# Kernel optimization log

Measured on AMD Instinct MI355X. Metric: run time of the kernel, lower is better.

Reference implementation:

```python
import jax, jax.numpy as jnp
import numpy as np

D_MODEL = 1024


def setup_inputs() -> dict:
    key = jax.random.key(0)
    ks = jax.random.split(key, 9)
    B, S, D = 4, 2048, D_MODEL
    scale = 1.0 / np.sqrt(D)
    inp = {
        "tokens": jax.random.normal(ks[0], (B, S, D), dtype=jnp.float32),
        "Wq": jax.random.normal(ks[1], (D, D), dtype=jnp.float32) * scale,
        "bq": jnp.zeros((D,), dtype=jnp.float32),
        "Wk": jax.random.normal(ks[2], (D, D), dtype=jnp.float32) * scale,
        "bk": jnp.zeros((D,), dtype=jnp.float32),
        "Wv": jax.random.normal(ks[3], (D, D), dtype=jnp.float32) * scale,
        "bv": jnp.zeros((D,), dtype=jnp.float32),
        "Wo": jax.random.normal(ks[4], (D, D), dtype=jnp.float32) * scale,
        "bo": jnp.zeros((D,), dtype=jnp.float32),
    }
    return inp


def reference(tokens, Wq, bq, Wk, bk, Wv, bv, Wo, bo):
    # use_activation=True, use_residual=True
    residual = tokens
    x = jax.nn.gelu(tokens, approximate=False)  # F.gelu default is exact (erf)
    q = jnp.einsum("bsd,de->bse", x, Wq) + bq
    k = jnp.einsum("bsd,de->bse", x, Wk) + bk
    v = jnp.einsum("bsd,de->bse", x, Wv) + bv
    scale = 1.0 / jnp.sqrt(jnp.asarray(tokens.shape[-1], dtype=tokens.dtype))
    scores = jnp.einsum("bqd,bkd->bqk", q, k) * scale  # [B,S,S]
    attn = jax.nn.softmax(scores, axis=-1)
    mixed = jnp.einsum("bqk,bkd->bqd", attn, v)
    out = jnp.einsum("bsd,de->bse", mixed, Wo) + bo
    return out + residual
```

## Files before the change

kernel.cpp:

```cpp
#include <hip/hip_runtime.h>
#include <hip/hip_bf16.h>
#include <cstdint>
#include <cstddef>

typedef unsigned short u16;
using frag_ab = __attribute__((ext_vector_type(8))) short;
using f32x4   = __attribute__((ext_vector_type(4))) float;

__device__ __forceinline__ u16 f2bf(float x) {
    __hip_bfloat16 h = __float2bfloat16(x);
    return *reinterpret_cast<u16*>(&h);
}

__device__ __forceinline__ void gload_lds16(const u16* g, u16* l) {
    __builtin_amdgcn_global_load_lds(
        (const __attribute__((address_space(1))) uint32_t*)g,
        (__attribute__((address_space(3)))       uint32_t*)l,
        16, 0, 0);
}

#define WAITV4() do { asm volatile("s_waitcnt vmcnt(4)" ::: "memory"); \
                      __builtin_amdgcn_sched_barrier(0); } while (0)
#define WAITV0() do { asm volatile("s_waitcnt vmcnt(0)" ::: "memory"); \
                      __builtin_amdgcn_sched_barrier(0); } while (0)
#define BAR()    do { asm volatile("" ::: "memory"); __builtin_amdgcn_s_barrier(); \
                      __builtin_amdgcn_sched_barrier(0); } while (0)
#define LGKMC(N) do { asm volatile("s_waitcnt lgkmcnt(" #N ")" ::: "memory"); \
                      __builtin_amdgcn_sched_barrier(0); } while (0)
#define LGKM0()  LGKMC(0)

template<int EPI, int BN_>
__global__ __launch_bounds__(512, 2)
void gemm3a(const u16* __restrict__ A, const u16* __restrict__ Bt,
            void* __restrict__ C0,
            const float* __restrict__ b0, const float* __restrict__ resid,
            int K, int lda, int ldb, int ldc,
            long long sA, long long sB, long long sC, float alpha,
            float* __restrict__ partials, int nz)
{
    constexpr int NFQ  = BN_ / 64;
    constexpr int WN   = BN_ / 2;
    constexpr int BBUF = BN_ * 64;
    __shared__ __align__(16) u16 lds[49152 + 2 * BBUF];

    const int gx  = gridDim.x;
    const int gid = blockIdx.x + gx * blockIdx.y;
    const int c   = gid & 7;
    const int idx = gid >> 3;
    const int z   = c % nz;
    const int sub = c / nz;
    const int W   = gridDim.y >> 3;
    const int mp  = sub * W + idx % W;
    const int np  = idx / W;
    const int m0  = mp * 256;
    const int n0  = np * BN_;

    A  += (long long)z * sA;
    Bt += (long long)z * sB;

    const int t    = threadIdx.x;
    const int lane = t & 63;
    const int wave = t >> 6;
    const int wm   = wave >> 1;
    const int wn   = wave & 1;

    const int r0  = t >> 3;
    const int ssw = (t & 7) ^ (r0 & 7);
    const u16* gsA_0 = A  + (size_t)(m0 +       r0) * lda + ssw * 8;
    const u16* gsA_1 = A  + (size_t)(m0 +  64 + r0) * lda + ssw * 8;
    const u16* gsA_2 = A  + (size_t)(m0 + 128 + r0) * lda + ssw * 8;
    const u16* gsA_3 = A  + (size_t)(m0 + 192 + r0) * lda + ssw * 8;
    const u16* gsB_0 = Bt + (size_t)(n0 +       r0) * ldb + ssw * 8;
    const u16* gsB_1 = Bt + (size_t)(n0 +  64 + r0) * ldb + ssw * 8;
    const u16* gsB_2 = (BN_ == 256) ? Bt + (size_t)(n0 + 128 + r0) * ldb + ssw * 8 : gsB_0;
    const u16* gsB_3 = (BN_ == 256) ? Bt + (size_t)(n0 + 192 + r0) * ldb + ssw * 8 : gsB_1;

#define STA(BUF, H, KT) do {                                                   \
    gload_lds16(((H) ? gsA_2 : gsA_0) + (size_t)(KT) * 64,                     \
                lds + (BUF) * 16384 + (H) * 8192 + t * 8);                     \
    gload_lds16(((H) ? gsA_3 : gsA_1) + (size_t)(KT) * 64,                     \
                lds + (BUF) * 16384 + (H) * 8192 + 4096 + t * 8);              \
} while (0)
#define STB(BUF, H, KT) do {                                                   \
    gload_lds16(((H) ? gsB_2 : gsB_0) + (size_t)(KT) * 64,                     \
                lds + 49152 + (BUF) * BBUF + (H) * 8192 + t * 8);              \
    gload_lds16(((H) ? gsB_3 : gsB_1) + (size_t)(KT) * 64,                     \
                lds + 49152 + (BUF) * BBUF + (H) * 8192 + 4096 + t * 8);       \
} while (0)

    const int ar   = lane & 15;
    const int ko   = lane >> 4;
    const int aoff = (wm * 64 + ar) * 64;
    const int boff = 49152 + (wn * WN + ar) * 64;
    const int as0  = ((0 + ko) ^ (ar & 7)) * 8;
    const int as1  = ((4 + ko) ^ (ar & 7)) * 8;

    frag_ab areg[2][2];
    frag_ab breg[2][NFQ][2];
    f32x4   acc[4][2 * NFQ] = {};

#define RDA3(AB, MQ) do { _Pragma("unroll") for (int mf = 0; mf < 2; ++mf) {   \
    areg[mf][0] = *(const frag_ab*)(lds + (AB) + aoff + ((MQ)*2+mf)*1024 + as0); \
    areg[mf][1] = *(const frag_ab*)(lds + (AB) + aoff + ((MQ)*2+mf)*1024 + as1); } } while (0)

#define RDB3(BO, NQ) do { _Pragma("unroll") for (int jf = 0; jf < NFQ; ++jf) { \
    breg[NQ][jf][0] = *(const frag_ab*)(lds + (BO) + boff + ((NQ)*NFQ+jf)*1024 + as0); \
    breg[NQ][jf][1] = *(const frag_ab*)(lds + (BO) + boff + ((NQ)*NFQ+jf)*1024 + as1); } } while (0)

#define MMAQ3(MQ, NQ) do { __builtin_amdgcn_s_setprio(1);                      \
    _Pragma("unroll") for (int mf = 0; mf < 2; ++mf)                           \
    _Pragma("unroll") for (int jf = 0; jf < NFQ; ++jf) {                       \
        acc[(MQ)*2+mf][(NQ)*NFQ+jf] = __builtin_amdgcn_mfma_f32_16x16x32_bf16( \
            areg[mf][0], breg[NQ][jf][0], acc[(MQ)*2+mf][(NQ)*NFQ+jf], 0,0,0); \
        acc[(MQ)*2+mf][(NQ)*NFQ+jf] = __builtin_amdgcn_mfma_f32_16x16x32_bf16( \
            areg[mf][1], breg[NQ][jf][1], acc[(MQ)*2+mf][(NQ)*NFQ+jf], 0,0,0); \
    } __builtin_amdgcn_s_setprio(0); } while (0)

    const int nk = K / 64;
    STA(0, 0, 0); STA(0, 1, 0);
    STB(0, 0, 0);
    if constexpr (BN_ == 256) STB(0, 1, 0);
    STA(1, 0, 1); STA(1, 1, 1);
    WAITV4();
    BAR();

    int ab = 0, bb = 0;
    for (int tt = 0; tt < nk; ++tt) {
        const int ab2 = (ab + 2 >= 3) ? ab - 1 : ab + 2;
        const int bb1 = bb ^ 1;
        const int tB  = (tt + 1 < nk) ? tt + 1 : nk - 1;
        const int tA  = (tt + 2 < nk) ? tt + 2 : nk - 1;
        const int AB = ab * 16384, BB = bb * BBUF;
        RDA3(AB, 0); RDB3(BB, 0);
        STB(bb1, 0, tB);
        if constexpr (BN_ == 256) LGKMC(8);
        BAR(); LGKM0(); MMAQ3(0, 0);
        RDB3(BB, 1);
        if constexpr (BN_ == 256) STB(bb1, 1, tB);
        BAR(); LGKM0(); MMAQ3(0, 1);
        RDA3(AB, 1);
        STA(ab2, 0, tA);
        BAR(); LGKM0(); MMAQ3(1, 0);
        STA(ab2, 1, tA);
        WAITV4();
        BAR(); MMAQ3(1, 1);
        ab = (ab + 1 >= 3) ? 0 : ab + 1;
        bb = bb1;
    }

    const int cr = (lane >> 4) * 4;
    const int cc = lane & 15;

    float* fl = (float*)lds;
    if constexpr (EPI == 2) {
        WAITV0();
        BAR();
        if (t < 256) {
            const float* p = partials + ((size_t)z * 2048 + m0 + t) * 16;
            float s = 0.0f;
            #pragma unroll
            for (int i = 0; i < 16; ++i) s += p[i];
            fl[t] = 1.0f / s;
        }
        BAR();
    }

    float rs[4][4];
    if constexpr (EPI == 1) {
        #pragma unroll
        for (int mi = 0; mi < 4; ++mi)
            #pragma unroll
            for (int r = 0; r < 4; ++r) rs[mi][r] = 0.0f;
    }

    #pragma unroll
    for (int mi = 0; mi < 4; ++mi) {
        const int rowb = m0 + wm * 64 + mi * 16 + cr;
        const int rloc = wm * 64 + mi * 16 + cr;
        #pragma unroll
        for (int gj = 0; gj < 2 * NFQ; ++gj) {
            const int col = n0 + wn * WN + gj * 16 + cc;
            if constexpr (EPI == 0) {
                const int plane = col >> 10;
                const int cl    = col & 1023;
                const float bvv = ((plane == 0) ? b0 : resid)[cl];
                u16* Cw = (u16*)C0 + (size_t)plane * sC;
                #pragma unroll
                for (int r = 0; r < 4; ++r)
                    Cw[(size_t)(rowb + r) * ldc + cl] = f2bf(acc[mi][gj][r] + bvv);
            } else {
                const float bvv = (EPI == 3) ? b0[col] : 0.0f;
                #pragma unroll
                for (int r = 0; r < 4; ++r) {
                    const size_t row = (size_t)(rowb + r);
                    float v = acc[mi][gj][r];
                    if (EPI == 1) { v = __expf(v * alpha); rs[mi][r] += v; }
                    if (EPI == 2) v *= fl[rloc + r];
                    v += bvv;
                    if (EPI == 3) {
                        v += resid[row * ldc + col];
                        ((float*)C0)[(size_t)z * sC + row * ldc + col] = v;
                    } else {
                        ((u16*)C0)[(size_t)z * sC + row * ldc + col] = f2bf(v);
                    }
                }
            }
        }
    }

    if constexpr (EPI == 1) {
        #pragma unroll
        for (int mi = 0; mi < 4; ++mi)
            #pragma unroll
            for (int r = 0; r < 4; ++r) {
                float s = rs[mi][r];
                s += __shfl_xor(s, 1); s += __shfl_xor(s, 2);
                s += __shfl_xor(s, 4); s += __shfl_xor(s, 8);
                rs[mi][r] = s;
            }
        if (cc == 0) {
            const int chunk = (n0 >> 7) + wn;
            #pragma unroll
            for (int mi = 0; mi < 4; ++mi) {
                const int rowb = m0 + wm * 64 + mi * 16 + cr;
                #pragma unroll
                for (int r = 0; r < 4; ++r)
                    partials[((size_t)z * 2048 + rowb + r) * 16 + chunk] = rs[mi][r];
            }
        }
    }
#undef STA
#undef STB
#undef RDA3
#undef RDB3
#undef MMAQ3
}

__global__ __launch_bounds__(256, 2)
void gemm128_v(const u16* __restrict__ A, const u16* __restrict__ Bt,
               u16* __restrict__ VT, const float* __restrict__ bv,
               int K, int lda, int ldb)
{
    constexpr int BUFSTR = 16384;
    __shared__ __align__(16) u16 lds[2 * BUFSTR];

    const int gx  = gridDim.x;
    const int nwg = gx * gridDim.y;
    const int cpx = nwg >> 3;
    int lin = blockIdx.x + gx * blockIdx.y;
    lin = (lin & 7) * cpx + (lin >> 3);
    const int m0 = (lin / gx) * 128;
    const int n0 = (lin % gx) * 128;

    const int t    = threadIdx.x;
    const int lane = t & 63;
    const int wave = t >> 6;
    const int wm   = wave >> 1;
    const int wn   = wave & 1;

    const int r0  = t >> 3;
    const int ssw = (t & 7) ^ (r0 & 7);
    const u16* gsA0_0 = A  + (size_t)(m0 +       r0) * lda + ssw * 8;
    const u16* gsA0_1 = A  + (size_t)(m0 +  32 + r0) * lda + ssw * 8;
    const u16* gsA1_0 = A  + (size_t)(m0 +  64 + r0) * lda + ssw * 8;
    const u16* gsA1_1 = A  + (size_t)(m0 +  96 + r0) * lda + ssw * 8;
    const u16* gsB0_0 = Bt + (size_t)(n0 +       r0) * ldb + ssw * 8;
    const u16* gsB0_1 = Bt + (size_t)(n0 +  32 + r0) * ldb + ssw * 8;
    const u16* gsB1_0 = Bt + (size_t)(n0 +  64 + r0) * ldb + ssw * 8;
    const u16* gsB1_1 = Bt + (size_t)(n0 +  96 + r0) * ldb + ssw * 8;

#define OPO_A 0
#define OPO_B 8192
#define STAGE(BI, OP, H, KT) do {                                              \
    gload_lds16(gs##OP##H##_0 + (size_t)(KT) * 64,                             \
                lds + (BI) * BUFSTR + OPO_##OP + (H) * 4096 + t * 8);          \
    gload_lds16(gs##OP##H##_1 + (size_t)(KT) * 64,                             \
                lds + (BI) * BUFSTR + OPO_##OP + (H) * 4096 + 2048 + t * 8);   \
} while (0)

    const int ar   = lane & 15;
    const int ko   = lane >> 4;
    const int aoff = (wm * 64 + ar) * 64;
    const int boff = OPO_B + (wn * 64 + ar) * 64;
    const int as0  = ((0 + ko) ^ (ar & 7)) * 8;
    const int as1  = ((4 + ko) ^ (ar & 7)) * 8;

    frag_ab areg[2][2];
    frag_ab breg[2][2][2];
    f32x4   acc[4][4] = {};

#define RDA(BI, MQ) do { _Pragma("unroll") for (int mf = 0; mf < 2; ++mf) {    \
    areg[mf][0] = *(const frag_ab*)(lds + (BI)*BUFSTR + aoff + ((MQ)*2+mf)*1024 + as0); \
    areg[mf][1] = *(const frag_ab*)(lds + (BI)*BUFSTR + aoff + ((MQ)*2+mf)*1024 + as1); } } while (0)

#define RDB(BI, NQ) do { _Pragma("unroll") for (int jf = 0; jf < 2; ++jf) {    \
    breg[NQ][jf][0] = *(const frag_ab*)(lds + (BI)*BUFSTR + boff + ((NQ)*2+jf)*1024 + as0); \
    breg[NQ][jf][1] = *(const frag_ab*)(lds + (BI)*BUFSTR + boff + ((NQ)*2+jf)*1024 + as1); } } while (0)

#define MMAQ(MQ, NQ) do { __builtin_amdgcn_s_setprio(1);                       \
    _Pragma("unroll") for (int mf = 0; mf < 2; ++mf)                           \
    _Pragma("unroll") for (int jf = 0; jf < 2; ++jf) {                         \
        acc[(MQ)*2+mf][(NQ)*2+jf] = __builtin_amdgcn_mfma_f32_16x16x32_bf16(   \
            areg[mf][0], breg[NQ][jf][0], acc[(MQ)*2+mf][(NQ)*2+jf], 0,0,0);   \
        acc[(MQ)*2+mf][(NQ)*2+jf] = __builtin_amdgcn_mfma_f32_16x16x32_bf16(   \
            areg[mf][1], breg[NQ][jf][1], acc[(MQ)*2+mf][(NQ)*2+jf], 0,0,0);   \
    } __builtin_amdgcn_s_setprio(0); } while (0)

    const int nk = K / 64;
    STAGE(0, A, 0, 0); STAGE(0, A, 1, 0); STAGE(0, B, 0, 0); STAGE(0, B, 1, 0);
    STAGE(1, B, 0, 1); STAGE(1, A, 0, 1);
    WAITV4();
    BAR();

    const int nIter = nk >> 1;
    for (int it = 0; it < nIter; ++it) {
        const int O  = 2 * it + 1;
        const int E2 = (2 * it + 2 < nk) ? 2 * it + 2 : nk - 1;
        const int O2 = (2 * it + 3 < nk) ? 2 * it + 3 : nk - 1;

        RDA(0, 0); RDB(0, 0); STAGE(1, A, 1, O);  BAR(); LGKM0(); MMAQ(0, 0);
        RDB(0, 1);            STAGE(1, B, 1, O);  BAR(); LGKM0(); MMAQ(0, 1);
        RDA(0, 1);            STAGE(0, B, 0, E2); BAR(); LGKM0(); MMAQ(1, 0);
        STAGE(0, A, 0, E2);   WAITV4();           BAR();          MMAQ(1, 1);
        RDA(1, 0); RDB(1, 0); STAGE(0, A, 1, E2); BAR(); LGKM0(); MMAQ(0, 0);
        RDB(1, 1);            STAGE(0, B, 1, E2); BAR(); LGKM0(); MMAQ(0, 1);
        RDA(1, 1);            STAGE(1, B, 0, O2); BAR(); LGKM0(); MMAQ(1, 0);
        STAGE(1, A, 0, O2);   WAITV4();           BAR();          MMAQ(1, 1);
    }

    const int cr = (lane >> 4) * 4;
    const int cc = lane & 15;

    WAITV0();
    BAR();
    constexpr int TP = 136;
    u16* T = lds;
    #pragma unroll
    for (int mi = 0; mi < 4; ++mi) {
        const int rloc = wm * 64 + mi * 16 + cr;
        #pragma unroll
        for (int gj = 0; gj < 4; ++gj) {
            const int cl = wn * 64 + gj * 16 + cc;
            const float bvv = bv[n0 + cl];
            union { u16 u[4]; uint2 q; } pk;
            #pragma unroll
            for (int r = 0; r < 4; ++r) pk.u[r] = f2bf(acc[mi][gj][r] + bvv);
            *(uint2*)&T[cl * TP + rloc] = pk.q;
        }
    }
    BAR();
    const int bb   = m0 >> 11;
    const int s0   = m0 & 2047;
    const int d    = t >> 1;
    const int half = t & 1;
    const u16* src = T + d * TP + half * 64;
    u16* dg = VT + (size_t)bb * 1024 * 2048 + (size_t)(n0 + d) * 2048 + s0 + half * 64;
    #pragma unroll
    for (int j = 0; j < 8; ++j)
        ((uint4*)dg)[j] = ((const uint4*)src)[j];
#undef STAGE
#undef RDA
#undef RDB
#undef MMAQ
#undef OPO_A
#undef OPO_B
}

__global__ __launch_bounds__(256)
void prep_kernel(const float4* __restrict__ in, uint4* __restrict__ outp,
                 const float* __restrict__ W0, const float* __restrict__ W1,
                 const float* __restrict__ W2, const float* __restrict__ W3,
                 u16* __restrict__ WT, int D, int NG)
{
    __shared__ float tile[32][33];
    const int b = blockIdx.x;
    const int t = threadIdx.x;
    if (b < NG) {
        const int i = (b * 256 + t) * 2;
        float4 x0 = in[i], x1 = in[i + 1];
        auto g = [](float v) { return 0.5f * v * (1.0f + erff(v * 0.70710678118654752f)); };
        union { u16 u[8]; uint4 q; } pk;
        pk.u[0] = f2bf(g(x0.x)); pk.u[1] = f2bf(g(x0.y));
        pk.u[2] = f2bf(g(x0.z)); pk.u[3] = f2bf(g(x0.w));
        pk.u[4] = f2bf(g(x1.x)); pk.u[5] = f2bf(g(x1.y));
        pk.u[6] = f2bf(g(x1.z)); pk.u[7] = f2bf(g(x1.w));
        outp[b * 256 + t] = pk.q;
        return;
    }
    const int j   = b - NG;
    const int z   = j >> 10;
    const int rem = j & 1023;
    const int n0  = (rem & 31) * 32;
    const int k0  = (rem >> 5) * 32;
    const float* W = (z == 0) ? W0 : (z == 1) ? W1 : (z == 2) ? W2 : W3;
    u16* o = WT + (size_t)z * D * D;
    const int tx = t & 31, ty = t >> 5;
    #pragma unroll
    for (int r = 0; r < 4; ++r)
        tile[ty + 8 * r][tx] = W[(size_t)(k0 + ty + 8 * r) * D + n0 + tx];
    __syncthreads();
    const int tx16 = t & 15, ny = t >> 4;
    #pragma unroll
    for (int r = 0; r < 2; ++r) {
        const int nl = ny + 16 * r;
        union { u16 u[2]; unsigned q; } pk;
        pk.u[0] = f2bf(tile[2 * tx16][nl]);
        pk.u[1] = f2bf(tile[2 * tx16 + 1][nl]);
        ((unsigned*)(o + (size_t)(n0 + nl) * D + k0))[tx16] = pk.q;
    }
}

extern "C" void kernel_launch(void* const* d_in, const int* in_sizes, int n_in,
                              void* d_out, int out_size, void* d_ws, size_t ws_size,
                              hipStream_t stream)
{
    const int B = 4, S = 2048, D = 1024;
    const int M = B * S;

    const float* tokens = (const float*)d_in[0];
    const float* Wq = (const float*)d_in[1];
    const float* bq = (const float*)d_in[2];
    const float* Wk = (const float*)d_in[3];
    const float* bk = (const float*)d_in[4];
    const float* Wv = (const float*)d_in[5];
    const float* bv = (const float*)d_in[6];
    const float* Wo = (const float*)d_in[7];
    const float* bo = (const float*)d_in[8];
    float* out = (float*)d_out;

    char* ws = (char*)d_ws;
    size_t o = 0;
    u16* x_bf = (u16*)(ws + o); o += (size_t)M * D * 2;
    u16* wT   = (u16*)(ws + o); o += (size_t)4 * D * D * 2;
    u16* q_bf = (u16*)(ws + o); o += (size_t)M * D * 2;
    u16* k_bf = (u16*)(ws + o); o += (size_t)M * D * 2;
    u16* vt   = (u16*)(ws + o); o += (size_t)M * D * 2;
    u16*   E        = (u16*)(ws + o);   o += (size_t)B * S * S * 2;
    float* partials = (float*)(ws + o); o += (size_t)B * S * 16 * 4;
    u16* mixed = x_bf;

    const int NG = M * D / 8 / 256;
    prep_kernel<<<dim3(NG + 4096), dim3(256), 0, stream>>>(
        (const float4*)tokens, (uint4*)x_bf, Wq, Wk, Wv, Wo, wT, D, NG);

    gemm3a<0, 256><<<dim3(2 * D / 256, M / 256, 1), dim3(512), 0, stream>>>(
        x_bf, wT, q_bf, bq, bk,
        D, D, D, D, 0, 0, (long long)M * D, 1.0f, nullptr, 1);

    gemm128_v<<<dim3(D / 128, M / 128, 1), dim3(256), 0, stream>>>(
        x_bf, wT + 2 * D * D, vt, bv, D, D, D);

    gemm3a<1, 256><<<dim3(S / 256, 32, 1), dim3(512), 0, stream>>>(
        q_bf, k_bf, E, nullptr, nullptr,
        D, D, D, S, (long long)S * D, (long long)S * D, (long long)S * S, 0.03125f,
        partials, 4);

    gemm3a<2, 128><<<dim3(D / 128, 32, 1), dim3(512), 0, stream>>>(
        E, vt, mixed, nullptr, nullptr,
        S, S, S, D, (long long)S * S, (long long)D * S, (long long)S * D, 1.0f,
        partials, 4);

    gemm3a<3, 128><<<dim3(D / 128, M / 256, 1), dim3(512), 0, stream>>>(
        mixed, wT + 3 * D * D, out, bo, tokens,
        D, D, D, D, 0, 0, 0, 1.0f, nullptr, 1);
}
```

Baseline: 164.1 us.

## Double-buffer A fragments and prefetch next-tile LDS reads ahead of MFMA

Splits the A-fragment registers into two sets and reorders the GEMM main loop so each LDS fragment read is issued before the preceding MFMA block and waited on afterward, overlapping LDS latency with matrix math. The first-quadrant fragments for the next K tile are read before the final MFMA block of the current tile, with a prologue read added before the loop. This costs extra VGPRs for the second A set, which may reduce occupancy or cause spills, and it depends on the barrier placement still protecting the buffers being overwritten.

```diff
diff --git a/kernel.cpp b/kernel.cpp
--- a/kernel.cpp
+++ b/kernel.cpp
@@ -95,25 +95,26 @@
     const int as0  = ((0 + ko) ^ (ar & 7)) * 8;
     const int as1  = ((4 + ko) ^ (ar & 7)) * 8;
 
-    frag_ab areg[2][2];
+    frag_ab aregA[2][2];
+    frag_ab aregB[2][2];
     frag_ab breg[2][NFQ][2];
     f32x4   acc[4][2 * NFQ] = {};
 
-#define RDA3(AB, MQ) do { _Pragma("unroll") for (int mf = 0; mf < 2; ++mf) {   \
-    areg[mf][0] = *(const frag_ab*)(lds + (AB) + aoff + ((MQ)*2+mf)*1024 + as0); \
-    areg[mf][1] = *(const frag_ab*)(lds + (AB) + aoff + ((MQ)*2+mf)*1024 + as1); } } while (0)
+#define RDA3(DST, AB, MQ) do { _Pragma("unroll") for (int mf = 0; mf < 2; ++mf) { \
+    DST[mf][0] = *(const frag_ab*)(lds + (AB) + aoff + ((MQ)*2+mf)*1024 + as0); \
+    DST[mf][1] = *(const frag_ab*)(lds + (AB) + aoff + ((MQ)*2+mf)*1024 + as1); } } while (0)
 
 #define RDB3(BO, NQ) do { _Pragma("unroll") for (int jf = 0; jf < NFQ; ++jf) { \
     breg[NQ][jf][0] = *(const frag_ab*)(lds + (BO) + boff + ((NQ)*NFQ+jf)*1024 + as0); \
     breg[NQ][jf][1] = *(const frag_ab*)(lds + (BO) + boff + ((NQ)*NFQ+jf)*1024 + as1); } } while (0)
 
-#define MMAQ3(MQ, NQ) do { __builtin_amdgcn_s_setprio(1);                      \
+#define MMAQ3(ASET, MQ, NQ) do { __builtin_amdgcn_s_setprio(1);                \
     _Pragma("unroll") for (int mf = 0; mf < 2; ++mf)                           \
     _Pragma("unroll") for (int jf = 0; jf < NFQ; ++jf) {                       \
         acc[(MQ)*2+mf][(NQ)*NFQ+jf] = __builtin_amdgcn_mfma_f32_16x16x32_bf16( \
-            areg[mf][0], breg[NQ][jf][0], acc[(MQ)*2+mf][(NQ)*NFQ+jf], 0,0,0); \
+            ASET[mf][0], breg[NQ][jf][0], acc[(MQ)*2+mf][(NQ)*NFQ+jf], 0,0,0); \
         acc[(MQ)*2+mf][(NQ)*NFQ+jf] = __builtin_amdgcn_mfma_f32_16x16x32_bf16( \
-            areg[mf][1], breg[NQ][jf][1], acc[(MQ)*2+mf][(NQ)*NFQ+jf], 0,0,0); \
+            ASET[mf][1], breg[NQ][jf][1], acc[(MQ)*2+mf][(NQ)*NFQ+jf], 0,0,0); \
     } __builtin_amdgcn_s_setprio(0); } while (0)
 
     const int nk = K / 64;
@@ -123,28 +124,31 @@
     STA(1, 0, 1); STA(1, 1, 1);
     WAITV4();
     BAR();
+    RDA3(aregA, 0, 0); RDB3(0, 0);
+    LGKM0();
 
     int ab = 0, bb = 0;
     for (int tt = 0; tt < nk; ++tt) {
+        const int abn = (ab + 1 >= 3) ? 0 : ab + 1;
         const int ab2 = (ab + 2 >= 3) ? ab - 1 : ab + 2;
         const int bb1 = bb ^ 1;
         const int tB  = (tt + 1 < nk) ? tt + 1 : nk - 1;
         const int tA  = (tt + 2 < nk) ? tt + 2 : nk - 1;
-        const int AB = ab * 16384, BB = bb * BBUF;
-        RDA3(AB, 0); RDB3(BB, 0);
+        const int AB  = ab * 16384, BB = bb * BBUF;
+        const int ABn = abn * 16384, BBn = bb1 * BBUF;
+        RDB3(BB, 1);
         STB(bb1, 0, tB);
-        if constexpr (BN_ == 256) LGKMC(8);
-        BAR(); LGKM0(); MMAQ3(0, 0);
-        RDB3(BB, 1);
+        BAR(); MMAQ3(aregA, 0, 0); LGKM0();
+        RDA3(aregB, AB, 1);
         if constexpr (BN_ == 256) STB(bb1, 1, tB);
-        BAR(); LGKM0(); MMAQ3(0, 1);
-        RDA3(AB, 1);
+        BAR(); MMAQ3(aregA, 0, 1); LGKM0();
         STA(ab2, 0, tA);
-        BAR(); LGKM0(); MMAQ3(1, 0);
+        BAR(); MMAQ3(aregB, 1, 0); LGKM0();
         STA(ab2, 1, tA);
         WAITV4();
-        BAR(); MMAQ3(1, 1);
-        ab = (ab + 1 >= 3) ? 0 : ab + 1;
+        RDA3(aregA, ABn, 0); RDB3(BBn, 0);
+        BAR(); MMAQ3(aregB, 1, 1); LGKM0();
+        ab = abn;
         bb = bb1;
     }
 
```

New measurement: 165.6 us. Within noise of the previous version (+0.9%).
